# Optimization experiments

Measured on AMD Instinct MI355X. Metric: run time of the kernel, lower is better.

The kernel has to match this reference:

```python
import jax, jax.numpy as jnp
import numpy as np

NUM_HEADS = 16
DIM_HEADS = 64
DIM_INPUT = 1024
DIM = NUM_HEADS * DIM_HEADS  # 1024


def setup_inputs() -> dict:
    key = jax.random.key(0)
    ks = jax.random.split(key, 8)
    B, S = 2, 2048
    inputs = jax.random.normal(ks[0], (B, S, DIM_INPUT), dtype=jnp.float32)
    attention_mask = jnp.zeros((B, 1, 1, S), dtype=jnp.float32)
    s = 1.0 / np.sqrt(DIM_INPUT)
    Wq = jax.random.normal(ks[1], (DIM_INPUT, DIM), dtype=jnp.float32) * s
    bq = jnp.zeros((DIM,), dtype=jnp.float32)
    Wk = jax.random.normal(ks[2], (DIM_INPUT, DIM), dtype=jnp.float32) * s
    bk = jnp.zeros((DIM,), dtype=jnp.float32)
    Wv = jax.random.normal(ks[3], (DIM_INPUT, DIM), dtype=jnp.float32) * s
    bv = jnp.zeros((DIM,), dtype=jnp.float32)
    return {"inputs": inputs, "attention_mask": attention_mask,
            "Wq": Wq, "bq": bq, "Wk": Wk, "bk": bk, "Wv": Wv, "bv": bv}


def _split_heads(x):
    # [B, S, H*dh] -> [B, H, S, dh]
    B, S, _ = x.shape
    return x.reshape(B, S, NUM_HEADS, DIM_HEADS).transpose(0, 2, 1, 3)


def reference(inputs, attention_mask, Wq, bq, Wk, bk, Wv, bv):
    q = _split_heads(inputs @ Wq + bq)  # [B,H,S,dh]
    k = _split_heads(inputs @ Wk + bk)
    v = _split_heads(inputs @ Wv + bv)
    scores = jnp.einsum('bhsd,bhtd->bhst', q, k) / np.sqrt(DIM_HEADS).astype(np.float32)
    scores = scores + attention_mask  # broadcast additive mask
    probs = jax.nn.softmax(scores, axis=-1)  # dropout is identity in eval
    ctx = jnp.einsum('bhst,bhtd->bhsd', probs, v)  # [B,H,S,dh]
    B, H, S, dh = ctx.shape
    return ctx.transpose(0, 2, 1, 3).reshape(B, S, H * dh)
```

## Files before the change

### kernel.cpp

```cpp
#include <hip/hip_runtime.h>


typedef __attribute__((ext_vector_type(4))) float f32x4;
typedef __attribute__((ext_vector_type(16))) float f32x16;
typedef __attribute__((ext_vector_type(8))) __bf16 bf16x8;

#define DEV static __device__ __forceinline__

constexpr int S_ = 2048;
constexpr int H_ = 16;
constexpr int DH_ = 64;
constexpr int DIN_ = 1024;
constexpr int M_ = 2 * S_;
constexpr int N3_ = 3 * 1024;
constexpr int K_ = DIN_;
constexpr float LOG2E = 1.44269504088896340736f;

DEV unsigned short f2bf(float f) {
  unsigned u = __builtin_bit_cast(unsigned, f);
  u += 0x7fffu + ((u >> 16) & 1u);
  return (unsigned short)(u >> 16);
}

DEV unsigned cvt_pk(float lo, float hi) {
  unsigned d;
  asm("v_cvt_pk_bf16_f32 %0, %1, %2" : "=v"(d) : "v"(lo), "v"(hi));
  return d;
}

DEV void gload_lds16(const void* g, void* l) {
  __builtin_amdgcn_global_load_lds(
      (const __attribute__((address_space(1))) unsigned int*)g,
      (__attribute__((address_space(3))) unsigned int*)l, 16, 0, 0);
}

DEV int kswz(int row, int colb) { return row * 128 + (colb ^ ((row & 7) << 4)); }

__global__ __launch_bounds__(256) void convert_x(const float* __restrict__ X,
                                                 unsigned short* __restrict__ Xbf) {
  int idx = (blockIdx.x * 256 + threadIdx.x) * 8;
  float4 a = *(const float4*)(X + idx);
  float4 b = *(const float4*)(X + idx + 4);
  unsigned short r[8];
  r[0] = f2bf(a.x); r[1] = f2bf(a.y); r[2] = f2bf(a.z); r[3] = f2bf(a.w);
  r[4] = f2bf(b.x); r[5] = f2bf(b.y); r[6] = f2bf(b.z); r[7] = f2bf(b.w);
  *(uint4*)(Xbf + idx) = *(uint4*)r;
}

__global__ __launch_bounds__(256) void transpose_w(const float* __restrict__ Wq,
                                                   const float* __restrict__ Wk,
                                                   const float* __restrict__ Wv,
                                                   unsigned short* __restrict__ Wt) {
  __shared__ float tile[32][33];
  int z = blockIdx.z;
  const float* W = (z == 0) ? Wq : (z == 1) ? Wk : Wv;
  int n0 = blockIdx.x * 32, k0 = blockIdx.y * 32;
  int tx = threadIdx.x, ty = threadIdx.y;
  for (int i = 0; i < 4; ++i)
    tile[ty + i * 8][tx] = W[(size_t)(k0 + ty + i * 8) * 1024 + n0 + tx];
  __syncthreads();
  for (int i = 0; i < 4; ++i)
    Wt[(size_t)(z * 1024 + n0 + ty + i * 8) * 1024 + k0 + tx] =
        f2bf(tile[tx][ty + i * 8]);
}

__global__ __launch_bounds__(256) void qkv_gemm(
    const unsigned short* __restrict__ Xbf, const unsigned short* __restrict__ Wt,
    const float* __restrict__ bq, const float* __restrict__ bk,
    const float* __restrict__ bv, unsigned short* __restrict__ Qw,
    unsigned short* __restrict__ Kw, unsigned short* __restrict__ Vt) {
  __shared__ unsigned short Abuf[128 * 32];
  __shared__ unsigned short Bbuf[128 * 32];
  int tid = threadIdx.x;
  int w = tid >> 6, l = tid & 63;
  int row16 = l & 15, kg = l >> 4;
  int mBase = blockIdx.y * 128, nBase = blockIdx.x * 128;
  int wm = w >> 1, wn = w & 1;

  f32x4 acc[4][4] = {};

  int srow = l >> 2;
  int scol = (l & 3) * 8;

  for (int kt = 0; kt < K_ / 32; ++kt) {
    int k0 = kt * 32;
    __syncthreads();
    for (int i = 0; i < 2; ++i) {
      int c = w * 2 + i;
      int r = c * 16 + srow;
      gload_lds16(Xbf + (size_t)(mBase + r) * K_ + k0 + scol,
                  (char*)Abuf + c * 1024);
      gload_lds16(Wt + (size_t)(nBase + r) * K_ + k0 + scol,
                  (char*)Bbuf + c * 1024);
    }
    __syncthreads();
    bf16x8 af[4], bfr[4];
#pragma unroll
    for (int m = 0; m < 4; ++m)
      af[m] = *(const bf16x8*)&Abuf[(wm * 64 + m * 16 + row16) * 32 + kg * 8];
#pragma unroll
    for (int n = 0; n < 4; ++n)
      bfr[n] = *(const bf16x8*)&Bbuf[(wn * 64 + n * 16 + row16) * 32 + kg * 8];
#pragma unroll
    for (int m = 0; m < 4; ++m)
#pragma unroll
      for (int n = 0; n < 4; ++n)
        acc[m][n] = __builtin_amdgcn_mfma_f32_16x16x32_bf16(af[m], bfr[n],
                                                            acc[m][n], 0, 0, 0);
  }

#pragma unroll
  for (int n = 0; n < 4; ++n) {
    int gn = nBase + wn * 64 + n * 16 + row16;
    int which = gn >> 10;
    int nn = gn & 1023;
    float bias = (which == 0 ? bq : which == 1 ? bk : bv)[nn];
    unsigned short* dst = (which == 0) ? Qw : (which == 1) ? Kw : Vt;
    float scl = (which == 0) ? 0.125f * LOG2E : 1.0f;
    int hh = nn >> 6, dd = nn & 63;
#pragma unroll
    for (int m = 0; m < 4; ++m) {
      int gm0 = mBase + wm * 64 + m * 16 + kg * 4;
#pragma unroll
      for (int j = 0; j < 4; ++j) {
        int gm = gm0 + j;
        int bb = gm >> 11, ss = gm & 2047;
        float v = (acc[m][n][j] + bias) * scl;
        size_t idx;
        if (which == 2)
          idx = ((size_t)(bb * H_ + hh) * DH_ + dd) * S_ + ss;
        else
          idx = ((size_t)(bb * H_ + hh) * S_ + ss) * DH_ + dd;
        dst[idx] = f2bf(v);
      }
    }
  }
}

__global__ __launch_bounds__(256) void attn_fwd(
    const unsigned short* __restrict__ Qw, const unsigned short* __restrict__ Kw,
    const unsigned short* __restrict__ Vt, const float* __restrict__ mask,
    float* __restrict__ out) {
  __shared__ __align__(16) unsigned short Ks[2][64 * 64];
  __shared__ __align__(16) unsigned short Vs[2][64 * 64];
  __shared__ float Ms[S_];

  const int tid = threadIdx.x;
  const int w = tid >> 6, l = tid & 63;
  const int lq = l & 31;
  const int h = l >> 5;
  const int bh = blockIdx.y, b = bh >> 4, hh = bh & 15;
  const int q0 = blockIdx.x * 128 + w * 32;

  const unsigned short* Kb = Kw + (size_t)bh * S_ * DH_;
  const unsigned short* Vb = Vt + (size_t)bh * DH_ * S_;

  for (int i = tid * 4; i < S_; i += 256 * 4) {
    float4 mv = *(const float4*)(mask + (size_t)b * S_ + i);
    mv.x *= LOG2E; mv.y *= LOG2E; mv.z *= LOG2E; mv.w *= LOG2E;
    *(float4*)&Ms[i] = mv;
  }

  bf16x8 qf[4];
  {
    const unsigned short* qrow = Qw + ((size_t)bh * S_ + q0 + lq) * DH_;
#pragma unroll
    for (int kk = 0; kk < 4; ++kk)
      qf[kk] = *(const bf16x8*)(qrow + kk * 16 + h * 8);
  }

  const int srow = tid >> 3;
  const int tc8 = (tid & 7) * 8;
  const int wk0 = kswz(srow, (tid & 7) * 16);

  bf16x8 kr0 = *(const bf16x8*)(Kb + (size_t)srow * DH_ + tc8);
  bf16x8 kr1 = *(const bf16x8*)(Kb + (size_t)(srow + 32) * DH_ + tc8);
  bf16x8 vr0 = *(const bf16x8*)(Vb + (size_t)srow * S_ + tc8);
  bf16x8 vr1 = *(const bf16x8*)(Vb + (size_t)(srow + 32) * S_ + tc8);
  {
    char* KsB = (char*)Ks[0];
    char* VsB = (char*)Vs[0];
    *(bf16x8*)(KsB + wk0) = kr0;
    *(bf16x8*)(KsB + wk0 + 4096) = kr1;
    *(bf16x8*)(VsB + wk0) = vr0;
    *(bf16x8*)(VsB + wk0 + 4096) = vr1;
  }
  kr0 = *(const bf16x8*)(Kb + (size_t)(64 + srow) * DH_ + tc8);
  kr1 = *(const bf16x8*)(Kb + (size_t)(96 + srow) * DH_ + tc8);
  vr0 = *(const bf16x8*)(Vb + (size_t)srow * S_ + 64 + tc8);
  vr1 = *(const bf16x8*)(Vb + (size_t)(srow + 32) * S_ + 64 + tc8);
  __syncthreads();

  float l_run = 0.f;
  f32x16 O0 = {}, O1 = {};

  constexpr int NT = S_ / 64;
  for (int it = 0; it < NT; ++it) {
    const int t0 = it * 64;
    const int cur = it & 1;
    char* KsB = (char*)Ks[cur];
    char* VsB = (char*)Vs[cur];

    if (it < NT - 1) {
      char* KsN = (char*)Ks[cur ^ 1];
      char* VsN = (char*)Vs[cur ^ 1];
      *(bf16x8*)(KsN + wk0) = kr0;
      *(bf16x8*)(KsN + wk0 + 4096) = kr1;
      *(bf16x8*)(VsN + wk0) = vr0;
      *(bf16x8*)(VsN + wk0 + 4096) = vr1;
      if (it < NT - 2) {
        const int tn = t0 + 128;
        kr0 = *(const bf16x8*)(Kb + (size_t)(tn + srow) * DH_ + tc8);
        kr1 = *(const bf16x8*)(Kb + (size_t)(tn + 32 + srow) * DH_ + tc8);
        vr0 = *(const bf16x8*)(Vb + (size_t)srow * S_ + tn + tc8);
        vr1 = *(const bf16x8*)(Vb + (size_t)(srow + 32) * S_ + tn + tc8);
      }
    }

    f32x16 p0, p1;
#pragma unroll
    for (int r2 = 0; r2 < 4; ++r2) {
      f32x4 a = *(const f32x4*)&Ms[t0 + r2 * 8 + h * 4];
      f32x4 bq4 = *(const f32x4*)&Ms[t0 + 32 + r2 * 8 + h * 4];
#pragma unroll
      for (int c = 0; c < 4; ++c) { p0[4 * r2 + c] = a[c]; p1[4 * r2 + c] = bq4[c]; }
    }

    __builtin_amdgcn_s_setprio(1);
#pragma unroll
    for (int kk = 0; kk < 4; ++kk) {
      bf16x8 kf = *(const bf16x8*)(KsB + kswz(lq, kk * 32 + h * 16));
      p0 = __builtin_amdgcn_mfma_f32_32x32x16_bf16(kf, qf[kk], p0, 0, 0, 0);
    }
#pragma unroll
    for (int kk = 0; kk < 4; ++kk) {
      bf16x8 kf = *(const bf16x8*)(KsB + kswz(32 + lq, kk * 32 + h * 16));
      p1 = __builtin_amdgcn_mfma_f32_32x32x16_bf16(kf, qf[kk], p1, 0, 0, 0);
    }
    __builtin_amdgcn_s_setprio(0);

#pragma unroll
    for (int i = 0; i < 16; ++i) {
      p0[i] = __builtin_amdgcn_exp2f(p0[i]);
      p1[i] = __builtin_amdgcn_exp2f(p1[i]);
    }

    float s8[8];
#pragma unroll
    for (int i = 0; i < 8; ++i)
      s8[i] = (p0[i] + p0[i + 8]) + (p1[i] + p1[i + 8]);
    float rs = ((s8[0] + s8[1]) + (s8[2] + s8[3])) +
               ((s8[4] + s8[5]) + (s8[6] + s8[7]));
    rs += __shfl_xor(rs, 32, 64);
    l_run += rs;

    unsigned w0[8], w1[8];
#pragma unroll
    for (int r2 = 0; r2 < 4; ++r2) {
      w0[2 * r2]     = cvt_pk(p0[4 * r2 + 0], p0[4 * r2 + 1]);
      w0[2 * r2 + 1] = cvt_pk(p0[4 * r2 + 2], p0[4 * r2 + 3]);
      w1[2 * r2]     = cvt_pk(p1[4 * r2 + 0], p1[4 * r2 + 1]);
      w1[2 * r2 + 1] = cvt_pk(p1[4 * r2 + 2], p1[4 * r2 + 3]);
    }

    __builtin_amdgcn_s_setprio(1);
#pragma unroll
    for (int s = 0; s < 4; ++s) {
      const unsigned* W = (s < 2) ? w0 : w1;
      const int base = (s & 1) * 4;
      unsigned send0 = h ? W[base + 0] : W[base + 2];
      unsigned send1 = h ? W[base + 1] : W[base + 3];
      unsigned c0 = (unsigned)__shfl_xor((int)send0, 32, 64);
      unsigned c1 = (unsigned)__shfl_xor((int)send1, 32, 64);
      uint4 fw;
      fw.x = h ? c0 : W[base + 0];
      fw.y = h ? c1 : W[base + 1];
      fw.z = h ? W[base + 2] : c0;
      fw.w = h ? W[base + 3] : c1;
      bf16x8 pf = __builtin_bit_cast(bf16x8, fw);
      bf16x8 vf0 = *(const bf16x8*)(VsB + kswz(lq, s * 32 + h * 16));
      O0 = __builtin_amdgcn_mfma_f32_32x32x16_bf16(vf0, pf, O0, 0, 0, 0);
      bf16x8 vf1 = *(const bf16x8*)(VsB + kswz(32 + lq, s * 32 + h * 16));
      O1 = __builtin_amdgcn_mfma_f32_32x32x16_bf16(vf1, pf, O1, 0, 0, 0);
    }
    __builtin_amdgcn_s_setprio(0);

    __syncthreads();
  }

  float inv = 1.0f / l_run;
  float* orow = out + ((size_t)b * S_ + q0 + lq) * 1024 + hh * 64;
#pragma unroll
  for (int r2 = 0; r2 < 4; ++r2) {
    f32x4 v0, v1;
#pragma unroll
    for (int c = 0; c < 4; ++c) {
      v0[c] = O0[4 * r2 + c] * inv;
      v1[c] = O1[4 * r2 + c] * inv;
    }
    *(f32x4*)&orow[r2 * 8 + h * 4] = v0;
    *(f32x4*)&orow[32 + r2 * 8 + h * 4] = v1;
  }
}

extern "C" void kernel_launch(void* const* d_in, const int* in_sizes, int n_in,
                              void* d_out, int out_size, void* d_ws, size_t ws_size,
                              hipStream_t stream) {
  const float* X = (const float*)d_in[0];
  const float* mask = (const float*)d_in[1];
  const float* Wq = (const float*)d_in[2];
  const float* bq = (const float*)d_in[3];
  const float* Wk = (const float*)d_in[4];
  const float* bk = (const float*)d_in[5];
  const float* Wv = (const float*)d_in[6];
  const float* bv = (const float*)d_in[7];
  float* out = (float*)d_out;

  char* ws = (char*)d_ws;
  unsigned short* Xbf = (unsigned short*)ws;
  unsigned short* Wt  = (unsigned short*)(ws + (size_t)(8 << 20));
  unsigned short* Qw  = (unsigned short*)(ws + (size_t)(14 << 20));
  unsigned short* Kw  = (unsigned short*)(ws + (size_t)(22 << 20));
  unsigned short* Vt  = (unsigned short*)(ws + (size_t)(30 << 20));

  convert_x<<<dim3(M_ * K_ / (256 * 8)), dim3(256), 0, stream>>>(X, Xbf);
  transpose_w<<<dim3(32, 32, 3), dim3(32, 8), 0, stream>>>(Wq, Wk, Wv, Wt);
  qkv_gemm<<<dim3(N3_ / 128, M_ / 128), dim3(256), 0, stream>>>(
      Xbf, Wt, bq, bk, bv, Qw, Kw, Vt);
  attn_fwd<<<dim3(S_ / 128, 2 * H_), dim3(256), 0, stream>>>(Qw, Kw, Vt, mask, out);
}
```

Before: 110.3 us.

## Deepen GEMM K-tile to 64 and remap attention blocks for XCD locality

The QKV GEMM now stages a 64-wide K slice per iteration instead of 32. That halves the number of barrier pairs and doubles the MFMA work between syncs. The attention kernel switches to a 1D grid and remaps block IDs so that all query tiles of one batch-head land on the same XCD, which should improve K/V reuse in each XCD's L2. It also adds a launch_bounds occupancy hint of 2 blocks per CU. The larger LDS tiles raise shared memory use, and the new LDS row stride of 64 elements may introduce bank conflicts.

```diff
diff --git a/kernel.cpp b/kernel.cpp
--- a/kernel.cpp
+++ b/kernel.cpp
@@ -69,8 +69,8 @@
     const float* __restrict__ bq, const float* __restrict__ bk,
     const float* __restrict__ bv, unsigned short* __restrict__ Qw,
     unsigned short* __restrict__ Kw, unsigned short* __restrict__ Vt) {
-  __shared__ unsigned short Abuf[128 * 32];
-  __shared__ unsigned short Bbuf[128 * 32];
+  __shared__ unsigned short Abuf[128 * 64];
+  __shared__ unsigned short Bbuf[128 * 64];
   int tid = threadIdx.x;
   int w = tid >> 6, l = tid & 63;
   int row16 = l & 15, kg = l >> 4;
@@ -79,34 +79,40 @@
 
   f32x4 acc[4][4] = {};
 
-  int srow = l >> 2;
-  int scol = (l & 3) * 8;
-
-  for (int kt = 0; kt < K_ / 32; ++kt) {
-    int k0 = kt * 32;
+  const int grow = l >> 3;
+  const int gcol = (l & 7) * 8;
+
+  for (int kt = 0; kt < K_ / 64; ++kt) {
+    int k0 = kt * 64;
     __syncthreads();
-    for (int i = 0; i < 2; ++i) {
-      int c = w * 2 + i;
-      int r = c * 16 + srow;
-      gload_lds16(Xbf + (size_t)(mBase + r) * K_ + k0 + scol,
-                  (char*)Abuf + c * 1024);
-      gload_lds16(Wt + (size_t)(nBase + r) * K_ + k0 + scol,
-                  (char*)Bbuf + c * 1024);
+#pragma unroll
+    for (int j = 0; j < 4; ++j) {
+      int c1k = w * 4 + j;
+      int r = c1k * 8 + grow;
+      gload_lds16(Xbf + (size_t)(mBase + r) * K_ + k0 + gcol,
+                  (char*)Abuf + c1k * 1024);
+      gload_lds16(Wt + (size_t)(nBase + r) * K_ + k0 + gcol,
+                  (char*)Bbuf + c1k * 1024);
     }
     __syncthreads();
-    bf16x8 af[4], bfr[4];
-#pragma unroll
-    for (int m = 0; m < 4; ++m)
-      af[m] = *(const bf16x8*)&Abuf[(wm * 64 + m * 16 + row16) * 32 + kg * 8];
-#pragma unroll
-    for (int n = 0; n < 4; ++n)
-      bfr[n] = *(const bf16x8*)&Bbuf[(wn * 64 + n * 16 + row16) * 32 + kg * 8];
-#pragma unroll
-    for (int m = 0; m < 4; ++m)
+#pragma unroll
+    for (int kk = 0; kk < 2; ++kk) {
+      bf16x8 af[4], bfr[4];
+#pragma unroll
+      for (int m = 0; m < 4; ++m)
+        af[m] = *(const bf16x8*)&Abuf[(wm * 64 + m * 16 + row16) * 64 +
+                                      kk * 32 + kg * 8];
 #pragma unroll
       for (int n = 0; n < 4; ++n)
-        acc[m][n] = __builtin_amdgcn_mfma_f32_16x16x32_bf16(af[m], bfr[n],
-                                                            acc[m][n], 0, 0, 0);
+        bfr[n] = *(const bf16x8*)&Bbuf[(wn * 64 + n * 16 + row16) * 64 +
+                                       kk * 32 + kg * 8];
+#pragma unroll
+      for (int m = 0; m < 4; ++m)
+#pragma unroll
+        for (int n = 0; n < 4; ++n)
+          acc[m][n] = __builtin_amdgcn_mfma_f32_16x16x32_bf16(af[m], bfr[n],
+                                                              acc[m][n], 0, 0, 0);
+    }
   }
 
 #pragma unroll
@@ -137,7 +143,7 @@
   }
 }
 
-__global__ __launch_bounds__(256) void attn_fwd(
+__global__ __launch_bounds__(256, 2) void attn_fwd(
     const unsigned short* __restrict__ Qw, const unsigned short* __restrict__ Kw,
     const unsigned short* __restrict__ Vt, const float* __restrict__ mask,
     float* __restrict__ out) {
@@ -149,8 +155,12 @@
   const int w = tid >> 6, l = tid & 63;
   const int lq = l & 31;
   const int h = l >> 5;
-  const int bh = blockIdx.y, b = bh >> 4, hh = bh & 15;
-  const int q0 = blockIdx.x * 128 + w * 32;
+  const int wgid = blockIdx.x;
+  const int xcd = wgid & 7, ixd = wgid >> 3;
+  const int bh = xcd + 8 * (ixd >> 4);
+  const int qt = ixd & 15;
+  const int b = bh >> 4, hh = bh & 15;
+  const int q0 = qt * 128 + w * 32;
 
   const unsigned short* Kb = Kw + (size_t)bh * S_ * DH_;
   const unsigned short* Vb = Vt + (size_t)bh * DH_ * S_;
@@ -327,5 +337,5 @@
   transpose_w<<<dim3(32, 32, 3), dim3(32, 8), 0, stream>>>(Wq, Wk, Wv, Wt);
   qkv_gemm<<<dim3(N3_ / 128, M_ / 128), dim3(256), 0, stream>>>(
       Xbf, Wt, bq, bk, bv, Qw, Kw, Vt);
-  attn_fwd<<<dim3(S_ / 128, 2 * H_), dim3(256), 0, stream>>>(Qw, Kw, Vt, mask, out);
-}
+  attn_fwd<<<dim3(512), dim3(256), 0, stream>>>(Qw, Kw, Vt, mask, out);
+}
```

Measured after the change: 125.3 us. 1.14x slower.
